# Optimization experiments

Measured on AMD Instinct MI355X. Metric: run time of the kernel, lower is better.

## Reference

```python
import jax, jax.numpy as jnp
import numpy as np
import math

D_PAIR, D_BIAS, H, DH = 128, 128, 4, 32
B, L = 1, 384


def setup_inputs() -> dict:
    key = jax.random.key(0)
    ks = jax.random.split(key, 12)
    s = 0.02
    return {
        "pair": jax.random.normal(ks[0], (B, L, L, D_PAIR), jnp.float32),
        "bias": jax.random.normal(ks[1], (B, L, L, D_BIAS), jnp.float32),
        "ln_g": jnp.ones((D_PAIR,), jnp.float32),
        "ln_b": jnp.zeros((D_PAIR,), jnp.float32),
        "Wq": jax.random.normal(ks[2], (D_PAIR, H * DH), jnp.float32) * s,
        "Wk": jax.random.normal(ks[3], (D_PAIR, H * DH), jnp.float32) * s,
        "Wv": jax.random.normal(ks[4], (D_PAIR, H * DH), jnp.float32) * s,
        "Wb": jax.random.normal(ks[5], (D_BIAS, H), jnp.float32) * s,
        "Wg": jax.random.normal(ks[6], (D_PAIR, H * DH), jnp.float32) * s,
        "bg": jnp.ones((H * DH,), jnp.float32),
        "Wo": jax.random.normal(ks[7], (H * DH, D_PAIR), jnp.float32) * s,
        "bo": jnp.zeros((D_PAIR,), jnp.float32),
    }


def reference(pair, bias, ln_g, ln_b, Wq, Wk, Wv, Wb, Wg, bg, Wo, bo):
    # is_row=True: attend along the first L axis by permuting (i<->n)
    b_, l_ = pair.shape[:2]
    p = jnp.transpose(pair, (0, 2, 1, 3))  # [B,L,L,Dp]
    # LayerNorm over last dim (eps matches torch default)
    mu = jnp.mean(p, axis=-1, keepdims=True)
    var = jnp.mean(jnp.square(p - mu), axis=-1, keepdims=True)
    p = (p - mu) / jnp.sqrt(var + 1e-5) * ln_g + ln_b

    scaling = 1.0 / math.sqrt(DH)
    q = (p @ Wq).reshape(b_, l_, l_, H, DH) * scaling          # [B,n,i,h,c]
    k = (p @ Wk).reshape(b_, l_, l_, H, DH) / math.sqrt(l_)    # [B,n,j,h,c]
    # tied axial attention logits: sum over the n axis + projected bias
    logits = jnp.einsum("bnihc,bnjhc->bijh", q, k) + bias @ Wb  # [B,L,L,h]
    attn = jax.nn.softmax(logits, axis=-2)                      # softmax over j

    v = (p @ Wv).reshape(b_, l_, l_, H, DH)                     # [B,k,j,h,d]
    g = jax.nn.sigmoid(p @ Wg + bg)                             # [B,L,L,h*d]
    o = jnp.einsum("bijh,bkjhd->bikhd", attn, v).reshape(b_, l_, l_, H * DH)
    out = (g * o) @ Wo + bo                                     # [B,L,L,Dp]
    return jnp.transpose(out, (0, 2, 1, 3))  # undo is_row permute
```

## Files before the change

### kernel.cpp

```cpp
#include <hip/hip_runtime.h>
#include <math.h>

typedef unsigned short us;
typedef unsigned long long u64;
typedef short bf16x8 __attribute__((ext_vector_type(8)));
typedef short bf16x4 __attribute__((ext_vector_type(4)));
typedef float f32x4 __attribute__((ext_vector_type(4)));

#define LQ 384
#define DPAIR 128
#define KDIM 12288

#define WT_OFF   0UL
#define P_OFF    262144UL
#define LOG_OFF  262144UL
#define ATT_OFF  2621440UL
#define Q_OFF    38010880UL
#define K_OFF    75759616UL
#define V_OFF    113508352UL
#define G_OFF    151257088UL

__device__ __forceinline__ us f2bf(float x){
  unsigned u = __builtin_bit_cast(unsigned, x);
  return (us)((u + 0x7FFFu + ((u >> 16) & 1u)) >> 16);
}
__device__ __forceinline__ float bf2f(us b){
  unsigned u = ((unsigned)b) << 16;
  return __builtin_bit_cast(float, u);
}
__device__ __forceinline__ void gl_lds16(const void* g, void* l){
  __builtin_amdgcn_global_load_lds((const __attribute__((address_space(1))) unsigned*)g,
                                   (__attribute__((address_space(3))) unsigned*)l, 16, 0, 0);
}
__device__ __forceinline__ void nt_st8(us* p, bf16x8 v){
  __builtin_nontemporal_store(v, (bf16x8*)p);
}
__device__ __forceinline__ float wsum(float x){
  #pragma unroll
  for (int o = 32; o; o >>= 1) x += __shfl_xor(x, o, 64);
  return x;
}
__device__ __forceinline__ float wmaxr(float x){
  #pragma unroll
  for (int o = 32; o; o >>= 1) x = fmaxf(x, __shfl_xor(x, o, 64));
  return x;
}
__device__ __forceinline__ void stage_pair(const us* __restrict__ Arow, const us* __restrict__ Brow,
                                           size_t strideA, size_t strideB, int koff,
                                           us* ldsA, us* ldsB, int tid)
{
  #pragma unroll
  for (int s = 0; s < 4; ++s) {
    int slot = s * 256 + tid;
    int rrow = slot >> 3, cc = slot & 7;
    int cg = cc ^ (rrow & 7);
    gl_lds16(Arow + (size_t)rrow * strideA + koff + cg * 8, &ldsA[slot * 8]);
    gl_lds16(Brow + (size_t)rrow * strideB + koff + cg * 8, &ldsB[slot * 8]);
  }
}

__global__ __launch_bounds__(256) void k_prep(
    const float* __restrict__ Wq, const float* __restrict__ Wk,
    const float* __restrict__ Wv, const float* __restrict__ Wg,
    const float* __restrict__ Wo, us* __restrict__ wt,
    const float* __restrict__ pair, const float* __restrict__ lng,
    const float* __restrict__ lnb, us* __restrict__ P)
{
  const int bx = blockIdx.x;
  if (bx < 320) {
    int idx = bx * 256 + threadIdx.x;
    int m = idx >> 14, rr = idx & 16383, k = rr >> 7, n = rr & 127;
    const float* W; float s;
    switch (m) {
      case 0: W = Wq; s = 0.17677669529663687f; break;
      case 1: W = Wk; s = 0.05103103630798287f; break;
      case 2: W = Wv; s = 1.f; break;
      case 3: W = Wg; s = 1.f; break;
      default: W = Wo; s = 1.f; break;
    }
    wt[m * 16384 + n * 128 + k] = f2bf(W[k * 128 + n] * s);
    return;
  }
  const int tid = threadIdx.x, w = tid >> 6, l = tid & 63;
  const int gw = (bx - 320) * 4 + w;
  const int b = gw / 12, a0 = (gw % 12) * 32;
  const float2 lg = ((const float2*)lng)[l];
  const float2 lb = ((const float2*)lnb)[l];
  for (int it = 0; it < 8; ++it) {
    float2 x[4];
    #pragma unroll
    for (int rr = 0; rr < 4; ++rr) {
      int a = a0 + it * 4 + rr;
      x[rr] = ((const float2*)(pair + ((size_t)b * LQ + a) * DPAIR))[l];
    }
    #pragma unroll
    for (int rr = 0; rr < 4; ++rr) {
      int a = a0 + it * 4 + rr;
      float s = wsum(x[rr].x + x[rr].y);
      float q = wsum(x[rr].x * x[rr].x + x[rr].y * x[rr].y);
      float mu = s * (1.f / 128.f);
      float var = q * (1.f / 128.f) - mu * mu;
      float rstd = rsqrtf(var + 1e-5f);
      float y0 = (x[rr].x - mu) * rstd * lg.x + lb.x;
      float y1 = (x[rr].y - mu) * rstd * lg.y + lb.y;
      unsigned pk = (unsigned)f2bf(y0) | ((unsigned)f2bf(y1) << 16);
      ((unsigned*)(P + ((size_t)a * LQ + b) * DPAIR))[l] = pk;
    }
  }
}

__global__ __launch_bounds__(256, 4) void k_qkvg(
    const us* __restrict__ P, const us* __restrict__ wt,
    const float* __restrict__ bgp,
    us* __restrict__ Qw, us* __restrict__ Kw, us* __restrict__ Vw, us* __restrict__ Gw)
{
  __shared__ __attribute__((aligned(16))) us lds[17408];
  const int tid = threadIdx.x, w = tid >> 6, l = tid & 63;
  const int bx = blockIdx.x;
  const int xg = bx & 7, u = bx >> 3;
  int type, a_base, b0; bool qk;
  if (u < 288) {
    type = u & 1;
    int tq = xg * 144 + (u >> 1);
    a_base = (tq / 12) * 4; b0 = (tq % 12) * 32; qk = true;
  } else {
    int v = u - 288;
    type = 2 + (v & 1);
    int tv = xg * 144 + (v >> 1);
    a_base = tv / 3; b0 = (tv % 3) * 128; qk = false;
  }
  const us* W = wt + type * 16384;
  const int m0 = (w & 1) * 64, n0 = (w >> 1) * 64;
  const int row16 = l & 15, kq = l >> 4;

  #pragma unroll
  for (int s = 0; s < 8; ++s) {
    int slot = s * 256 + tid;
    int r = slot >> 4, c = slot & 15;
    int cg = (c & 8) | ((c & 7) ^ (r & 7));
    size_t prow = qk ? ((size_t)(a_base + (r >> 5)) * LQ + b0 + (r & 31))
                     : ((size_t)a_base * LQ + b0 + r);
    gl_lds16(P + prow * DPAIR + cg * 8, &lds[slot * 8]);
  }
  f32x4 acc[4][4];
  #pragma unroll
  for (int mt = 0; mt < 4; ++mt)
    #pragma unroll
    for (int nt = 0; nt < 4; ++nt) acc[mt][nt] = (f32x4){0.f, 0.f, 0.f, 0.f};
  asm volatile("s_waitcnt vmcnt(0)" ::: "memory");
  __syncthreads();

  #pragma unroll
  for (int kb = 0; kb < 4; ++kb) {
    bf16x8 bv[4], af[4];
    #pragma unroll
    for (int nt = 0; nt < 4; ++nt)
      bv[nt] = *(const bf16x8*)&W[(n0 + nt * 16 + row16) * DPAIR + kb * 32 + kq * 8];
    #pragma unroll
    for (int mt = 0; mt < 4; ++mt) {
      int r = m0 + mt * 16 + row16;
      int c = kb * 4 + kq;
      int cg = (c & 8) | ((c & 7) ^ (r & 7));
      af[mt] = *(const bf16x8*)&lds[r * 128 + cg * 8];
    }
    #pragma unroll
    for (int mt = 0; mt < 4; ++mt)
      #pragma unroll
      for (int nt = 0; nt < 4; ++nt)
        acc[mt][nt] = __builtin_amdgcn_mfma_f32_16x16x32_bf16(af[mt], bv[nt], acc[mt][nt], 0, 0, 0);
  }
  __syncthreads();

  if (qk) {
    us* T = lds;
    #pragma unroll
    for (int nt = 0; nt < 4; ++nt) {
      int n = n0 + nt * 16 + row16, h = n >> 5, cc = n & 31;
      #pragma unroll
      for (int mt = 0; mt < 4; ++mt) {
        f32x4 vv = acc[mt][nt];
        #pragma unroll
        for (int v4 = 0; v4 < 4; ++v4) {
          int r = m0 + mt * 16 + kq * 4 + v4;
          T[(h * 32 + (r & 31)) * 132 + (r >> 5) * 32 + cc] = f2bf(vv[v4]);
        }
      }
    }
    __syncthreads();
    us* dst = (type == 0) ? Qw : Kw;
    #pragma unroll
    for (int it = 0; it < 8; ++it) {
      int slot = it * 256 + tid;
      int combo = slot >> 4, chunk = slot & 15;
      int h = combo >> 5, bl = combo & 31;
      bf16x8 val = *(const bf16x8*)&T[combo * 132 + chunk * 8];
      nt_st8(&dst[((size_t)h * LQ + b0 + bl) * KDIM + a_base * 32 + chunk * 8], val);
    }
  } else if (type == 2) {
    us* T = lds;
    #pragma unroll
    for (int nt = 0; nt < 4; ++nt) {
      int col = n0 + nt * 16 + row16;
      #pragma unroll
      for (int mt = 0; mt < 4; ++mt) {
        int rowb = m0 + mt * 16 + kq * 4;
        f32x4 vv = acc[mt][nt];
        *(unsigned*)&T[col * 132 + rowb]     = (unsigned)f2bf(vv[0]) | ((unsigned)f2bf(vv[1]) << 16);
        *(unsigned*)&T[col * 132 + rowb + 2] = (unsigned)f2bf(vv[2]) | ((unsigned)f2bf(vv[3]) << 16);
      }
    }
    __syncthreads();
    #pragma unroll
    for (int it = 0; it < 8; ++it) {
      int slot = tid + 256 * it;
      int d = slot >> 4, jc = slot & 15;
      bf16x4 lo = *(const bf16x4*)&T[d * 132 + jc * 8];
      bf16x4 hi = *(const bf16x4*)&T[d * 132 + jc * 8 + 4];
      bf16x8 val = __builtin_shufflevector(lo, hi, 0, 1, 2, 3, 4, 5, 6, 7);
      int h = d >> 5, dd = d & 31;
      nt_st8(&Vw[((size_t)h * KDIM + a_base * 32 + dd) * LQ + b0 + jc * 8], val);
    }
  } else {
    us* Cs = lds;
    #pragma unroll
    for (int nt = 0; nt < 4; ++nt) {
      int col = n0 + nt * 16 + row16;
      float bgv = bgp[col];
      #pragma unroll
      for (int mt = 0; mt < 4; ++mt) {
        f32x4 vv = acc[mt][nt];
        #pragma unroll
        for (int v4 = 0; v4 < 4; ++v4) {
          float e = __expf(-(vv[v4] + bgv));
          Cs[(m0 + mt * 16 + kq * 4 + v4) * 136 + col] = f2bf(1.f / (1.f + e));
        }
      }
    }
    __syncthreads();
    #pragma unroll
    for (int it = 0; it < 8; ++it) {
      int slot = tid + 256 * it;
      int row = slot >> 4, chunk = slot & 15;
      bf16x8 val = *(const bf16x8*)&Cs[row * 136 + chunk * 8];
      nt_st8(&Gw[((size_t)(a_base * LQ + b0 + row)) * DPAIR + chunk * 8], val);
    }
  }
}

__global__ __launch_bounds__(256) void k_logits2(
    const us* __restrict__ Qw, const us* __restrict__ Kw,
    const float* __restrict__ bias, const float* __restrict__ Wb,
    float* __restrict__ logits)
{
  __shared__ __attribute__((aligned(16))) us AB[2][2][8192];
  const int tid = threadIdx.x, w = tid >> 6, l = tid & 63;
  const int bx = blockIdx.x;
  if (bx >= 576) {
    float* bps = (float*)AB;
    const int u2 = bx - 576;
    const int i = u2 / 3, j0 = (u2 % 3) * 128;
    const int g = l >> 4, sl = l & 15;
    const float4* Wb4 = (const float4*)Wb;
    float4 wb[8];
    #pragma unroll
    for (int e = 0; e < 8; ++e) wb[e] = Wb4[sl * 8 + e];
    for (int it = 0; it < 8; ++it) {
      int j = j0 + w * 32 + it * 4 + g;
      const float4* br = (const float4*)(bias + ((size_t)i * LQ + j) * DPAIR);
      float4 xa = br[sl * 2], xb = br[sl * 2 + 1];
      float p0 = 0.f, p1 = 0.f, p2 = 0.f, p3 = 0.f;
      #pragma unroll
      for (int e = 0; e < 4; ++e) {
        float xe = ((const float*)&xa)[e];
        p0 += xe * wb[e].x; p1 += xe * wb[e].y; p2 += xe * wb[e].z; p3 += xe * wb[e].w;
        float xf = ((const float*)&xb)[e];
        p0 += xf * wb[4 + e].x; p1 += xf * wb[4 + e].y; p2 += xf * wb[4 + e].z; p3 += xf * wb[4 + e].w;
      }
      #pragma unroll
      for (int o = 1; o < 16; o <<= 1) {
        p0 += __shfl_xor(p0, o, 64);
        p1 += __shfl_xor(p1, o, 64);
        p2 += __shfl_xor(p2, o, 64);
        p3 += __shfl_xor(p3, o, 64);
      }
      if (sl == 0) {
        int row = w * 32 + it * 4 + g;
        bps[row * 5 + 0] = p0; bps[row * 5 + 1] = p1; bps[row * 5 + 2] = p2; bps[row * 5 + 3] = p3;
      }
    }
    __syncthreads();
    #pragma unroll
    for (int rep = 0; rep < 2; ++rep) {
      int slot = rep * 256 + tid;
      int h = slot >> 7, jj = slot & 127;
      atomicAdd(&logits[((size_t)h * LQ + i) * LQ + j0 + jj], bps[jj * 5 + h]);
    }
    return;
  }
  const int xg = bx & 7, yg = bx >> 3;
  const int set = xg * 24 + yg / 3, j0 = (yg % 3) * 128;
  const int h = set / 48, rem = set % 48, i0 = (rem / 16) * 128, ks = rem % 16;
  const us* Ab = Qw + (size_t)h * LQ * KDIM + (size_t)i0 * KDIM;
  const us* Bb = Kw + (size_t)h * LQ * KDIM + (size_t)j0 * KDIM;
  f32x4 acc[4][4];
  #pragma unroll
  for (int mt = 0; mt < 4; ++mt)
    #pragma unroll
    for (int nt = 0; nt < 4; ++nt) acc[mt][nt] = (f32x4){0.f, 0.f, 0.f, 0.f};
  const int m0 = (w & 1) * 64, n0 = (w >> 1) * 64;
  const int row16 = l & 15, kq = l >> 4;
  stage_pair(Ab, Bb, KDIM, KDIM, ks * 768, AB[0][0], AB[0][1], tid);
  for (int kk = 0; kk < 12; ++kk) {
    const int cur = kk & 1;
    if (kk < 11) {
      stage_pair(Ab, Bb, KDIM, KDIM, ks * 768 + (kk + 1) * 64, AB[cur ^ 1][0], AB[cur ^ 1][1], tid);
      asm volatile("s_waitcnt vmcnt(8)" ::: "memory");
    } else {
      asm volatile("s_waitcnt vmcnt(0)" ::: "memory");
    }
    __syncthreads();
    #pragma unroll
    for (int kb = 0; kb < 2; ++kb) {
      bf16x8 af[4], bv[4];
      #pragma unroll
      for (int mt = 0; mt < 4; ++mt) {
        int r = m0 + mt * 16 + row16;
        int c = (kb * 4 + kq) ^ (r & 7);
        af[mt] = *(const bf16x8*)&AB[cur][0][r * 64 + c * 8];
      }
      #pragma unroll
      for (int nt = 0; nt < 4; ++nt) {
        int r = n0 + nt * 16 + row16;
        int c = (kb * 4 + kq) ^ (r & 7);
        bv[nt] = *(const bf16x8*)&AB[cur][1][r * 64 + c * 8];
      }
      #pragma unroll
      for (int mt = 0; mt < 4; ++mt)
        #pragma unroll
        for (int nt = 0; nt < 4; ++nt)
          acc[mt][nt] = __builtin_amdgcn_mfma_f32_16x16x32_bf16(af[mt], bv[nt], acc[mt][nt], 0, 0, 0);
    }
    __syncthreads();
  }
  #pragma unroll
  for (int mt = 0; mt < 4; ++mt)
    #pragma unroll
    for (int nt = 0; nt < 4; ++nt)
      #pragma unroll
      for (int v4 = 0; v4 < 4; ++v4) {
        int i = i0 + m0 + mt * 16 + kq * 4 + v4;
        int j = j0 + n0 + nt * 16 + row16;
        atomicAdd(&logits[((size_t)h * LQ + i) * LQ + j], acc[mt][nt][v4]);
      }
}

__global__ __launch_bounds__(256) void k_softmax(
    const float* __restrict__ logits, us* __restrict__ attn)
{
  const int tid = threadIdx.x, h = tid >> 6, l = tid & 63;
  const int i = blockIdx.x;
  const float* lrow = logits + ((size_t)h * LQ + i) * LQ;
  float x[6];
  #pragma unroll
  for (int s = 0; s < 6; ++s) x[s] = lrow[l + 64 * s];
  float mx = x[0];
  #pragma unroll
  for (int s = 1; s < 6; ++s) mx = fmaxf(mx, x[s]);
  mx = wmaxr(mx);
  float e[6], sum = 0.f;
  #pragma unroll
  for (int s = 0; s < 6; ++s) { e[s] = expf(x[s] - mx); sum += e[s]; }
  sum = wsum(sum);
  float rinv = 1.f / sum;
  #pragma unroll
  for (int s = 0; s < 6; ++s)
    attn[((size_t)h * LQ + i) * LQ + l + 64 * s] = f2bf(e[s] * rinv);
}

__global__ __launch_bounds__(256) void k_ogemm(
    const us* __restrict__ attn, const us* __restrict__ Vw, us* __restrict__ Gw)
{
  __shared__ __attribute__((aligned(16))) us AB[2][2][8192];
  const int tid = threadIdx.x, w = tid >> 6, l = tid & 63;
  const int bx = blockIdx.x;
  const int xg = bx & 7, yg = bx >> 3;
  const int set = xg * 48 + yg / 3, i0 = (yg % 3) * 128;
  const int h = set / 96, n0 = (set % 96) * 128;
  const us* Ab = attn + (size_t)h * LQ * LQ + (size_t)i0 * LQ;
  const us* Bb = Vw + (size_t)h * KDIM * LQ + (size_t)n0 * LQ;
  f32x4 acc[4][4];
  #pragma unroll
  for (int mt = 0; mt < 4; ++mt)
    #pragma unroll
    for (int nt = 0; nt < 4; ++nt) acc[mt][nt] = (f32x4){0.f, 0.f, 0.f, 0.f};
  const int m0 = (w & 1) * 64, n0w = (w >> 1) * 64;
  const int row16 = l & 15, kq = l >> 4;
  stage_pair(Ab, Bb, LQ, LQ, 0, AB[0][0], AB[0][1], tid);
  for (int kk = 0; kk < 6; ++kk) {
    const int cur = kk & 1;
    if (kk < 5) {
      stage_pair(Ab, Bb, LQ, LQ, (kk + 1) * 64, AB[cur ^ 1][0], AB[cur ^ 1][1], tid);
      asm volatile("s_waitcnt vmcnt(8)" ::: "memory");
    } else {
      asm volatile("s_waitcnt vmcnt(0)" ::: "memory");
    }
    __syncthreads();
    #pragma unroll
    for (int kb = 0; kb < 2; ++kb) {
      bf16x8 af[4], bv[4];
      #pragma unroll
      for (int mt = 0; mt < 4; ++mt) {
        int r = m0 + mt * 16 + row16;
        int c = (kb * 4 + kq) ^ (r & 7);
        af[mt] = *(const bf16x8*)&AB[cur][0][r * 64 + c * 8];
      }
      #pragma unroll
      for (int nt = 0; nt < 4; ++nt) {
        int r = n0w + nt * 16 + row16;
        int c = (kb * 4 + kq) ^ (r & 7);
        bv[nt] = *(const bf16x8*)&AB[cur][1][r * 64 + c * 8];
      }
      #pragma unroll
      for (int mt = 0; mt < 4; ++mt)
        #pragma unroll
        for (int nt = 0; nt < 4; ++nt)
          acc[mt][nt] = __builtin_amdgcn_mfma_f32_16x16x32_bf16(af[mt], bv[nt], acc[mt][nt], 0, 0, 0);
    }
    __syncthreads();
  }
  us* C = (us*)AB;
  #pragma unroll
  for (int mt = 0; mt < 4; ++mt)
    #pragma unroll
    for (int nt = 0; nt < 4; ++nt)
      #pragma unroll
      for (int v4 = 0; v4 < 4; ++v4)
        C[(m0 + mt * 16 + kq * 4 + v4) * 128 + n0w + nt * 16 + row16] = f2bf(acc[mt][nt][v4]);
  __syncthreads();
  const int k0 = n0 >> 5;
  #pragma unroll
  for (int it = 0; it < 8; ++it) {
    int slot = tid + 256 * it;
    int xr = slot >> 4, ch = slot & 15;
    bf16x8 ov = *(const bf16x8*)&C[xr * 128 + ch * 8];
    size_t eaddr = ((size_t)(i0 + xr) * LQ + k0 + (ch >> 2)) * DPAIR + h * 32 + (ch & 3) * 8;
    bf16x8 gv = *(const bf16x8*)&Gw[eaddr];
    bf16x8 ev;
    #pragma unroll
    for (int q = 0; q < 8; ++q)
      ev[q] = (short)f2bf(bf2f((us)(unsigned short)ov[q]) * bf2f((us)(unsigned short)gv[q]));
    *(bf16x8*)&Gw[eaddr] = ev;
  }
}

__global__ __launch_bounds__(256) void k_final(
    const us* __restrict__ E, const us* __restrict__ wt,
    const float* __restrict__ bo, float* __restrict__ out)
{
  __shared__ __attribute__((aligned(16))) us A[17408];
  const int tid = threadIdx.x, w = tid >> 6, l = tid & 63;
  const int y = blockIdx.x / 3, x0 = (blockIdx.x % 3) * 128;
  #pragma unroll
  for (int s4 = 0; s4 < 8; ++s4) {
    int slot = s4 * 256 + tid;
    int r = slot >> 4, c = slot & 15;
    int cg = (c & 8) | ((c & 7) ^ (r & 7));
    gl_lds16(E + ((size_t)(x0 + r) * LQ + y) * DPAIR + cg * 8, &A[slot * 8]);
  }
  asm volatile("s_waitcnt vmcnt(0)" ::: "memory");
  __syncthreads();
  const us* W = wt + 4 * 16384;
  const int m0 = (w & 1) * 64, n0w = (w >> 1) * 64;
  const int row16 = l & 15, kq = l >> 4;
  f32x4 acc[4][4];
  #pragma unroll
  for (int mt = 0; mt < 4; ++mt)
    #pragma unroll
    for (int nt = 0; nt < 4; ++nt) acc[mt][nt] = (f32x4){0.f, 0.f, 0.f, 0.f};
  #pragma unroll
  for (int kb = 0; kb < 4; ++kb) {
    bf16x8 af[4], bv[4];
    #pragma unroll
    for (int mt = 0; mt < 4; ++mt) {
      int r = m0 + mt * 16 + row16;
      int c = (kb * 4 + kq);
      int cg = (c & 8) | ((c & 7) ^ (r & 7));
      af[mt] = *(const bf16x8*)&A[r * 128 + cg * 8];
    }
    #pragma unroll
    for (int nt = 0; nt < 4; ++nt)
      bv[nt] = *(const bf16x8*)&W[(n0w + nt * 16 + row16) * 128 + kb * 32 + kq * 8];
    #pragma unroll
    for (int mt = 0; mt < 4; ++mt)
      #pragma unroll
      for (int nt = 0; nt < 4; ++nt)
        acc[mt][nt] = __builtin_amdgcn_mfma_f32_16x16x32_bf16(af[mt], bv[nt], acc[mt][nt], 0, 0, 0);
  }
  __syncthreads();
  float* Sf = (float*)A;
  #pragma unroll
  for (int half = 0; half < 2; ++half) {
    if ((w & 1) == half) {
      #pragma unroll
      for (int nt = 0; nt < 4; ++nt) {
        int col = n0w + nt * 16 + row16;
        float bov = bo[col];
        #pragma unroll
        for (int mt = 0; mt < 4; ++mt) {
          f32x4 vv = acc[mt][nt];
          #pragma unroll
          for (int v4 = 0; v4 < 4; ++v4)
            Sf[(mt * 16 + kq * 4 + v4) * 136 + col] = vv[v4] + bov;
        }
      }
    }
    __syncthreads();
    #pragma unroll
    for (int it = 0; it < 8; ++it) {
      int slot = it * 256 + tid;
      int rw = slot >> 5, ch = slot & 31;
      f32x4 v = *(const f32x4*)&Sf[rw * 136 + ch * 4];
      __builtin_nontemporal_store(v,
        (f32x4*)&out[((size_t)y * LQ + x0 + half * 64 + rw) * DPAIR + ch * 4]);
    }
    __syncthreads();
  }
}

extern "C" void kernel_launch(void* const* d_in, const int* in_sizes, int n_in,
                              void* d_out, int out_size, void* d_ws, size_t ws_size,
                              hipStream_t stream)
{
  const float* pair = (const float*)d_in[0];
  const float* bias = (const float*)d_in[1];
  const float* lng  = (const float*)d_in[2];
  const float* lnb  = (const float*)d_in[3];
  const float* Wq   = (const float*)d_in[4];
  const float* Wk   = (const float*)d_in[5];
  const float* Wv   = (const float*)d_in[6];
  const float* Wb   = (const float*)d_in[7];
  const float* Wg   = (const float*)d_in[8];
  const float* bg   = (const float*)d_in[9];
  const float* Wo   = (const float*)d_in[10];
  const float* bo   = (const float*)d_in[11];

  char* ws = (char*)d_ws;
  us* wt     = (us*)(ws + WT_OFF);
  us* P      = (us*)(ws + P_OFF);
  us* Qw     = (us*)(ws + Q_OFF);
  us* Kw     = (us*)(ws + K_OFF);
  us* Vw     = (us*)(ws + V_OFF);
  us* Gw     = (us*)(ws + G_OFF);
  us* attn   = (us*)(ws + ATT_OFF);
  float* logits = (float*)(ws + LOG_OFF);

  k_prep<<<1472, 256, 0, stream>>>(Wq, Wk, Wv, Wg, Wo, wt, pair, lng, lnb, P);
  k_qkvg<<<4608, 256, 0, stream>>>(P, wt, bg, Qw, Kw, Vw, Gw);
  (void)hipMemsetAsync(logits, 0, (size_t)4 * LQ * LQ * 4, stream);
  k_logits2<<<1728, 256, 0, stream>>>(Qw, Kw, bias, Wb, logits);
  k_softmax<<<384, 256, 0, stream>>>(logits, attn);
  k_ogemm<<<1152, 256, 0, stream>>>(attn, Vw, Gw);
  k_final<<<1152, 256, 0, stream>>>(Gw, wt, bo, (float*)d_out);
}
```

Baseline: 246.6 us.

## Store Q/K in natural row-major layout and gather per-head slices in logits GEMM

Q and K projections are now written in the same plain [a][b][128] layout as the gate output, dropping the LDS transpose into the head-major [h][i][n*32] layout. The projection kernel's tile scheduling is unified across all four weight types. The logits GEMM compensates with a new staging routine that gathers 64-byte per-head chunks from the row-major tensors, and its block mapping is reordered. This removes transpose work and scattered stores in the projection kernel, at the cost of less contiguous global loads in the logits kernel.

```diff
diff --git a/kernel.cpp b/kernel.cpp
--- a/kernel.cpp
+++ b/kernel.cpp
@@ -56,6 +56,18 @@
     int cg = cc ^ (rrow & 7);
     gl_lds16(Arow + (size_t)rrow * strideA + koff + cg * 8, &ldsA[slot * 8]);
     gl_lds16(Brow + (size_t)rrow * strideB + koff + cg * 8, &ldsB[slot * 8]);
+  }
+}
+__device__ __forceinline__ void stage_qk(const us* __restrict__ base, int i0, int koff, int h,
+                                         us* ldsDst, int tid)
+{
+  #pragma unroll
+  for (int s = 0; s < 4; ++s) {
+    int slot = s * 256 + tid;
+    int rrow = slot >> 3, cc = slot & 7;
+    int cg = cc ^ (rrow & 7);
+    int a_idx = (koff >> 5) + (cg >> 2), c_off = (cg & 3) * 8;
+    gl_lds16(base + ((size_t)a_idx * LQ + i0 + rrow) * DPAIR + h * 32 + c_off, &ldsDst[slot * 8]);
   }
 }
 
@@ -118,17 +130,9 @@
   const int tid = threadIdx.x, w = tid >> 6, l = tid & 63;
   const int bx = blockIdx.x;
   const int xg = bx & 7, u = bx >> 3;
-  int type, a_base, b0; bool qk;
-  if (u < 288) {
-    type = u & 1;
-    int tq = xg * 144 + (u >> 1);
-    a_base = (tq / 12) * 4; b0 = (tq % 12) * 32; qk = true;
-  } else {
-    int v = u - 288;
-    type = 2 + (v & 1);
-    int tv = xg * 144 + (v >> 1);
-    a_base = tv / 3; b0 = (tv % 3) * 128; qk = false;
-  }
+  const int type = u & 3;
+  const int tv = xg * 144 + (u >> 2);
+  const int a = tv / 3, b0 = (tv % 3) * 128;
   const us* W = wt + type * 16384;
   const int m0 = (w & 1) * 64, n0 = (w >> 1) * 64;
   const int row16 = l & 15, kq = l >> 4;
@@ -138,9 +142,7 @@
     int slot = s * 256 + tid;
     int r = slot >> 4, c = slot & 15;
     int cg = (c & 8) | ((c & 7) ^ (r & 7));
-    size_t prow = qk ? ((size_t)(a_base + (r >> 5)) * LQ + b0 + (r & 31))
-                     : ((size_t)a_base * LQ + b0 + r);
-    gl_lds16(P + prow * DPAIR + cg * 8, &lds[slot * 8]);
+    gl_lds16(P + ((size_t)a * LQ + b0 + r) * DPAIR + cg * 8, &lds[slot * 8]);
   }
   f32x4 acc[4][4];
   #pragma unroll
@@ -171,32 +173,7 @@
   }
   __syncthreads();
 
-  if (qk) {
-    us* T = lds;
-    #pragma unroll
-    for (int nt = 0; nt < 4; ++nt) {
-      int n = n0 + nt * 16 + row16, h = n >> 5, cc = n & 31;
-      #pragma unroll
-      for (int mt = 0; mt < 4; ++mt) {
-        f32x4 vv = acc[mt][nt];
-        #pragma unroll
-        for (int v4 = 0; v4 < 4; ++v4) {
-          int r = m0 + mt * 16 + kq * 4 + v4;
-          T[(h * 32 + (r & 31)) * 132 + (r >> 5) * 32 + cc] = f2bf(vv[v4]);
-        }
-      }
-    }
-    __syncthreads();
-    us* dst = (type == 0) ? Qw : Kw;
-    #pragma unroll
-    for (int it = 0; it < 8; ++it) {
-      int slot = it * 256 + tid;
-      int combo = slot >> 4, chunk = slot & 15;
-      int h = combo >> 5, bl = combo & 31;
-      bf16x8 val = *(const bf16x8*)&T[combo * 132 + chunk * 8];
-      nt_st8(&dst[((size_t)h * LQ + b0 + bl) * KDIM + a_base * 32 + chunk * 8], val);
-    }
-  } else if (type == 2) {
+  if (type == 2) {
     us* T = lds;
     #pragma unroll
     for (int nt = 0; nt < 4; ++nt) {
@@ -218,31 +195,33 @@
       bf16x4 hi = *(const bf16x4*)&T[d * 132 + jc * 8 + 4];
       bf16x8 val = __builtin_shufflevector(lo, hi, 0, 1, 2, 3, 4, 5, 6, 7);
       int h = d >> 5, dd = d & 31;
-      nt_st8(&Vw[((size_t)h * KDIM + a_base * 32 + dd) * LQ + b0 + jc * 8], val);
+      nt_st8(&Vw[((size_t)h * KDIM + a * 32 + dd) * LQ + b0 + jc * 8], val);
     }
   } else {
     us* Cs = lds;
     #pragma unroll
     for (int nt = 0; nt < 4; ++nt) {
       int col = n0 + nt * 16 + row16;
-      float bgv = bgp[col];
+      float bgv = (type == 3) ? bgp[col] : 0.f;
       #pragma unroll
       for (int mt = 0; mt < 4; ++mt) {
         f32x4 vv = acc[mt][nt];
         #pragma unroll
         for (int v4 = 0; v4 < 4; ++v4) {
-          float e = __expf(-(vv[v4] + bgv));
-          Cs[(m0 + mt * 16 + kq * 4 + v4) * 136 + col] = f2bf(1.f / (1.f + e));
+          float x = vv[v4];
+          if (type == 3) x = 1.f / (1.f + __expf(-(x + bgv)));
+          Cs[(m0 + mt * 16 + kq * 4 + v4) * 136 + col] = f2bf(x);
         }
       }
     }
     __syncthreads();
+    us* dst = (type == 0) ? Qw : (type == 1) ? Kw : Gw;
     #pragma unroll
     for (int it = 0; it < 8; ++it) {
       int slot = tid + 256 * it;
       int row = slot >> 4, chunk = slot & 15;
       bf16x8 val = *(const bf16x8*)&Cs[row * 136 + chunk * 8];
-      nt_st8(&Gw[((size_t)(a_base * LQ + b0 + row)) * DPAIR + chunk * 8], val);
+      nt_st8(&dst[((size_t)(a * LQ + b0 + row)) * DPAIR + chunk * 8], val);
     }
   }
 }
@@ -297,11 +276,11 @@
     }
     return;
   }
-  const int xg = bx & 7, yg = bx >> 3;
-  const int set = xg * 24 + yg / 3, j0 = (yg % 3) * 128;
-  const int h = set / 48, rem = set % 48, i0 = (rem / 16) * 128, ks = rem % 16;
-  const us* Ab = Qw + (size_t)h * LQ * KDIM + (size_t)i0 * KDIM;
-  const us* Bb = Kw + (size_t)h * LQ * KDIM + (size_t)j0 * KDIM;
+  const int xg = bx & 7, v = bx >> 3;
+  const int c6 = v / 12, jh = v % 12;
+  const int combo = c6 * 8 + xg;
+  const int i0 = (combo >> 4) * 128, ks = combo & 15;
+  const int j0 = (jh >> 2) * 128, h = jh & 3;
   f32x4 acc[4][4];
   #pragma unroll
   for (int mt = 0; mt < 4; ++mt)
@@ -309,11 +288,13 @@
     for (int nt = 0; nt < 4; ++nt) acc[mt][nt] = (f32x4){0.f, 0.f, 0.f, 0.f};
   const int m0 = (w & 1) * 64, n0 = (w >> 1) * 64;
   const int row16 = l & 15, kq = l >> 4;
-  stage_pair(Ab, Bb, KDIM, KDIM, ks * 768, AB[0][0], AB[0][1], tid);
+  stage_qk(Qw, i0, ks * 768, h, AB[0][0], tid);
+  stage_qk(Kw, j0, ks * 768, h, AB[0][1], tid);
   for (int kk = 0; kk < 12; ++kk) {
     const int cur = kk & 1;
     if (kk < 11) {
-      stage_pair(Ab, Bb, KDIM, KDIM, ks * 768 + (kk + 1) * 64, AB[cur ^ 1][0], AB[cur ^ 1][1], tid);
+      stage_qk(Qw, i0, ks * 768 + (kk + 1) * 64, h, AB[cur ^ 1][0], tid);
+      stage_qk(Kw, j0, ks * 768 + (kk + 1) * 64, h, AB[cur ^ 1][1], tid);
       asm volatile("s_waitcnt vmcnt(8)" ::: "memory");
     } else {
       asm volatile("s_waitcnt vmcnt(0)" ::: "memory");
```

Result: slower. 254.9 us (+3.3%).
